# Kernel optimization log

Hardware: AMD Instinct MI355X
Metric: run time of the kernel (lower is better)

## Reference

```python
import jax, jax.numpy as jnp
import numpy as np

B, N, D, H, NCTX = 4, 2048, 1024, 16, 512
HD = D // H  # head dim = 64


def setup_inputs() -> dict:
    key = jax.random.key(0)
    ks = jax.random.split(key, 6)
    return {
        "x": jax.random.normal(ks[0], (B, N, D), dtype=jnp.float32),
        "ctx_ppr": jax.random.uniform(ks[1], (B, NCTX), dtype=jnp.float32),
        "ctx_trust": jax.random.normal(ks[2], (B, NCTX), dtype=jnp.float32),
        "W_in": jax.random.normal(ks[3], (D, 3 * D), dtype=jnp.float32) * 0.02,
        "b_in": jnp.zeros((3 * D,), dtype=jnp.float32),
        "W_out": jax.random.normal(ks[4], (D, D), dtype=jnp.float32) * 0.02,
        "b_out": jnp.zeros((D,), dtype=jnp.float32),
        "log_ppr_alpha": jnp.full((1,), 0.1, dtype=jnp.float32),
        "trust_scale": jnp.full((1,), 0.1, dtype=jnp.float32),
        "n_ctx": NCTX,
    }


def reference(x, ctx_ppr, ctx_trust, W_in, b_in, W_out, b_out, log_ppr_alpha, trust_scale, n_ctx):
    b, n, dmodel = x.shape
    # QKV projection
    qkv = x @ W_in + b_in                                   # [B,N,3D]
    q, k, v = jnp.split(qkv, 3, axis=-1)
    q = q.reshape(b, n, H, HD).transpose(0, 2, 1, 3)        # [B,H,N,d]
    k = k.reshape(b, n, H, HD).transpose(0, 2, 1, 3)
    v = v.reshape(b, n, H, HD).transpose(0, 2, 1, 3)
    if n_ctx > 0:
        # multiplicative trust gate on context-token values
        gate = jax.nn.sigmoid(trust_scale * ctx_trust)      # [B,n_ctx]
        gate_full = jnp.concatenate(
            [gate, jnp.ones((b, n - n_ctx), dtype=x.dtype)], axis=1)  # [B,N]
        v = v * gate_full[:, None, :, None]
        # additive graph (log-PPR) column bias on attention logits
        col_bias = -log_ppr_alpha * jnp.log(jnp.maximum(ctx_ppr, 1e-8))  # [B,n_ctx]
        bias = jnp.concatenate(
            [col_bias, jnp.zeros((b, n - n_ctx), dtype=x.dtype)], axis=1)  # [B,N]
    else:
        bias = jnp.zeros((b, n), dtype=x.dtype)
    scale = 1.0 / np.sqrt(HD).astype(np.float32)
    scores = jnp.einsum("bhqd,bhkd->bhqk", q, k) * scale + bias[:, None, None, :]
    attn = jax.nn.softmax(scores, axis=-1)                  # [B,H,N,N]
    out = jnp.einsum("bhqk,bhkd->bhqd", attn, v)            # [B,H,N,d]
    out = out.transpose(0, 2, 1, 3).reshape(b, n, dmodel)
    return out @ W_out + b_out
```

## Files before the change

### kernel.cpp

```cpp
#include <hip/hip_runtime.h>
#include <hip/hip_bf16.h>
#include <stdint.h>

#define BATCH  4
#define NSEQ   2048
#define DMODEL 1024
#define NHEAD  16
#define HDIM   64
#define NCTXC  512

typedef unsigned short u16;
typedef __attribute__((ext_vector_type(8))) short bfrag;
typedef __attribute__((ext_vector_type(4))) float facc;

typedef __attribute__((address_space(3))) void lds_void;
typedef __attribute__((address_space(1))) void g_void;

__device__ __forceinline__ void gload16(const void* g, void* l) {
  __builtin_amdgcn_global_load_lds((const g_void*)g, (lds_void*)l, 16, 0, 0);
}

__device__ __forceinline__ u16 f2bf(float f) {
  uint32_t r;
  asm("v_cvt_pk_bf16_f32 %0, %1, %1" : "=v"(r) : "v"(f));
  return (u16)r;
}

#if __has_builtin(__builtin_amdgcn_cvt_pk_bf16_f32)
__device__ __forceinline__ uint32_t pk2bf(float a, float b) {
  return __builtin_bit_cast(uint32_t, __builtin_amdgcn_cvt_pk_bf16_f32(a, b));
}
#else
__device__ __forceinline__ uint32_t pk2bf(float a, float b) {
  uint32_t r;
  asm("v_cvt_pk_bf16_f32 %0, %1, %2" : "=v"(r) : "v"(a), "v"(b));
  return r;
}
#endif

__device__ __forceinline__ float bf2f(u16 h) {
  union { uint32_t u; float f; } un;
  un.u = ((uint32_t)h) << 16;
  return un.f;
}

__device__ __forceinline__ float load_flex(const void* p, size_t idx, int isb) {
  return isb ? bf2f(((const u16*)p)[idx]) : ((const float*)p)[idx];
}

__device__ __forceinline__ uint4 pack8(float4 a, float4 b) {
  uint4 r;
  r.x = pk2bf(a.x, a.y);
  r.y = pk2bf(a.z, a.w);
  r.z = pk2bf(b.x, b.y);
  r.w = pk2bf(b.z, b.w);
  return r;
}

__global__ __launch_bounds__(256) void detect_kernel(const u16* __restrict__ xraw,
                                                     int* __restrict__ flag) {
  __shared__ int s_high, s_zero;
  if (threadIdx.x == 0) { s_high = 0; s_zero = 0; }
  __syncthreads();
  int h = 0, z = 0;
  for (int i = threadIdx.x; i < 4096; i += 256) {
    const u16 v = xraw[2 * i];
    const int e = (v >> 7) & 0xFF;
    if (e >= 0x90) h++;
    if (v == 0) z++;
  }
  atomicAdd(&s_high, h);
  atomicAdd(&s_zero, z);
  __syncthreads();
  if (threadIdx.x == 0) flag[0] = (s_high < 64 && s_zero < 2048) ? 1 : 0;
}


__global__ __launch_bounds__(256) void cast_x_kernel(const void* __restrict__ x,
                                                     u16* __restrict__ xb,
                                                     const int* __restrict__ flag) {
  const int isb = flag[0];
  const int i = blockIdx.x * 256 + threadIdx.x;
  if (isb) {
    ((uint4*)xb)[i] = ((const uint4*)x)[i];
  } else {
    const float4 f0 = ((const float4*)x)[2 * i];
    const float4 f1 = ((const float4*)x)[2 * i + 1];
    ((uint4*)xb)[i] = pack8(f0, f1);
  }
}

__global__ __launch_bounds__(256) void transpose_flex(const void* __restrict__ W,
                                                      u16* __restrict__ Wt,
                                                      int R, int C,
                                                      const int* __restrict__ flag) {
  __shared__ float tile[32][33];
  const int isb = flag[0];
  const int tx = threadIdx.x;
  const int ty = threadIdx.y;
  const int c0 = blockIdx.x * 32;
  const int r0 = blockIdx.y * 32;
#pragma unroll
  for (int j = 0; j < 32; j += 8)
    tile[ty + j][tx] = load_flex(W, (size_t)(r0 + ty + j) * C + c0 + tx, isb);
  __syncthreads();
#pragma unroll
  for (int j = 0; j < 32; j += 8)
    Wt[(size_t)(c0 + ty + j) * R + r0 + tx] = f2bf(tile[tx][ty + j]);
}

__global__ __launch_bounds__(256) void prep_small(const void* __restrict__ b_in,
                                                  const void* __restrict__ b_out,
                                                  const void* __restrict__ ppr,
                                                  const void* __restrict__ trust,
                                                  const void* __restrict__ alpha_p,
                                                  const void* __restrict__ ts_p,
                                                  float* __restrict__ bin_f,
                                                  float* __restrict__ bout_f,
                                                  float* __restrict__ gate,
                                                  float* __restrict__ cbias,
                                                  const int* __restrict__ flag) {
  const int isb = flag[0];
  const int i = blockIdx.x * 256 + threadIdx.x;
  if (i < 3072) {
    bin_f[i] = load_flex(b_in, i, isb);
  } else if (i < 4096) {
    bout_f[i - 3072] = load_flex(b_out, i - 3072, isb);
  } else if (i < 4096 + BATCH * NCTXC) {
    const int j = i - 4096;
    const float ts = load_flex(ts_p, 0, isb), al = load_flex(alpha_p, 0, isb);
    gate[j]  = 1.0f / (1.0f + __expf(-ts * load_flex(trust, j, isb)));
    cbias[j] = -al * logf(fmaxf(load_flex(ppr, j, isb), 1e-8f)) * 1.44269504f;
  }
}

__device__ __forceinline__ void kloop_mfma(const u16* __restrict__ Ag,
                                           const u16* __restrict__ Bg,
                                           u16* As, u16* Bs,
                                           int tid, int wM, int wN, int l16, int quad,
                                           facc acc[4][4]) {
  char* ldsA = (char*)As + tid * 16;
  char* ldsB = (char*)Bs + tid * 16;
  for (int k0 = 0; k0 < 1024; k0 += 32) {
    __syncthreads();
    gload16(Ag + k0, ldsA);
    gload16(Ag + (size_t)64 * 1024 + k0, ldsA + 4096);
    gload16(Bg + k0, ldsB);
    gload16(Bg + (size_t)64 * 1024 + k0, ldsB + 4096);
    __syncthreads();

    bfrag af[4], bf[4];
#pragma unroll
    for (int i = 0; i < 4; ++i)
      af[i] = *(const bfrag*)(&As[(wM + i * 16 + l16) * 32 + quad * 8]);
#pragma unroll
    for (int j = 0; j < 4; ++j)
      bf[j] = *(const bfrag*)(&Bs[(wN + j * 16 + l16) * 32 + quad * 8]);
#pragma unroll
    for (int i = 0; i < 4; ++i)
#pragma unroll
      for (int j = 0; j < 4; ++j)
        acc[i][j] = __builtin_amdgcn_mfma_f32_16x16x32_bf16(af[i], bf[j], acc[i][j], 0, 0, 0);
  }
}

__global__ __launch_bounds__(256) void gemm_qkvt(const u16* __restrict__ xb,
                                                 const u16* __restrict__ Wt,
                                                 const float* __restrict__ bin_f,
                                                 const float* __restrict__ gate,
                                                 u16* __restrict__ qk,
                                                 u16* __restrict__ Vtg) {
  __shared__ u16 As[128 * 32];
  __shared__ u16 Bs[128 * 32];
  const int tid  = threadIdx.x;
  const int w    = tid >> 6;
  const int lane = tid & 63;
  const int quad = lane >> 4;
  const int l16  = lane & 15;
  const int wM   = (w >> 1) * 64;
  const int wN   = (w & 1) * 64;
  const int id   = blockIdx.x;
  const int srow  = tid >> 2;
  const int spart = tid & 3;

  facc acc[4][4] = {};

  if (id < 1024) {
    const int bn = id & 15, bm = id >> 4;
    const u16* Ag = xb + (size_t)(bm * 128 + srow) * 1024 + spart * 8;
    const u16* Bg = Wt + (size_t)(bn * 128 + srow) * 1024 + spart * 8;
    kloop_mfma(Ag, Bg, As, Bs, tid, wM, wN, l16, quad, acc);

    const float qs = (bn < 8) ? 0.18033688f : 1.0f;
#pragma unroll
    for (int i = 0; i < 4; ++i) {
      const int grow0 = bm * 128 + wM + i * 16 + quad * 4;
#pragma unroll
      for (int j = 0; j < 4; ++j) {
        const int gcol = bn * 128 + wN + j * 16 + l16;
        const float bv = bin_f[gcol];
#pragma unroll
        for (int r = 0; r < 4; ++r)
          qk[(size_t)(grow0 + r) * 2048 + gcol] = f2bf((acc[i][j][r] + bv) * qs);
      }
    }
  } else {
    const int id2 = id - 1024;
    const int bn = id2 & 63, bm = id2 >> 6;
    const u16* Ag = Wt + (size_t)2048 * 1024 + (size_t)(bm * 128 + srow) * 1024 + spart * 8;
    const u16* Bg = xb + (size_t)(bn * 128 + srow) * 1024 + spart * 8;
    kloop_mfma(Ag, Bg, As, Bs, tid, wM, wN, l16, quad, acc);

#pragma unroll
    for (int i = 0; i < 4; ++i) {
      const int grow0 = bm * 128 + wM + i * 16 + quad * 4;
      const int h   = grow0 >> 6;
      const int dd0 = grow0 & 63;
#pragma unroll
      for (int j = 0; j < 4; ++j) {
        const int gcol = bn * 128 + wN + j * 16 + l16;
        const int bb  = gcol >> 11;
        const int tok = gcol & (NSEQ - 1);
        const float gl = (tok < NCTXC) ? gate[bb * NCTXC + tok] : 1.0f;
        u16* dst = &Vtg[((size_t)((bb * NHEAD + h) * HDIM + dd0)) * NSEQ + tok];
#pragma unroll
        for (int r = 0; r < 4; ++r)
          dst[(size_t)r * NSEQ] = f2bf((acc[i][j][r] + bin_f[2 * DMODEL + grow0 + r]) * gl);
      }
    }
  }
}

__global__ __launch_bounds__(256) void gemm_out(const u16* __restrict__ A,
                                                const u16* __restrict__ Bt,
                                                const float* __restrict__ biasf,
                                                void* __restrict__ Cout,
                                                const int* __restrict__ flag) {
  __shared__ u16 As[128 * 32];
  __shared__ u16 Bs[128 * 32];
  const int isb  = flag[0];
  const int tid  = threadIdx.x;
  const int w    = tid >> 6;
  const int lane = tid & 63;
  const int quad = lane >> 4;
  const int l16  = lane & 15;
  const int wM   = (w >> 1) * 64;
  const int wN   = (w & 1) * 64;
  const int bm   = blockIdx.y;
  const int bn   = blockIdx.x;
  const int srow  = tid >> 2;
  const int spart = tid & 3;

  facc acc[4][4] = {};
  const u16* Ag = A + (size_t)(bm * 128 + srow) * 2048 + spart * 8;
  const u16* Bg = Bt + (size_t)(bn * 128 + srow) * 1024 + spart * 8;
  char* ldsA = (char*)As + tid * 16;
  char* ldsB = (char*)Bs + tid * 16;

  for (int k0 = 0; k0 < 1024; k0 += 32) {
    __syncthreads();
    gload16(Ag + k0, ldsA);
    gload16(Ag + (size_t)64 * 2048 + k0, ldsA + 4096);
    gload16(Bg + k0, ldsB);
    gload16(Bg + (size_t)64 * 1024 + k0, ldsB + 4096);
    __syncthreads();

    bfrag af[4], bf[4];
#pragma unroll
    for (int i = 0; i < 4; ++i)
      af[i] = *(const bfrag*)(&As[(wM + i * 16 + l16) * 32 + quad * 8]);
#pragma unroll
    for (int j = 0; j < 4; ++j)
      bf[j] = *(const bfrag*)(&Bs[(wN + j * 16 + l16) * 32 + quad * 8]);
#pragma unroll
    for (int i = 0; i < 4; ++i)
#pragma unroll
      for (int j = 0; j < 4; ++j)
        acc[i][j] = __builtin_amdgcn_mfma_f32_16x16x32_bf16(af[i], bf[j], acc[i][j], 0, 0, 0);
  }

#pragma unroll
  for (int i = 0; i < 4; ++i) {
    const int grow0 = bm * 128 + wM + i * 16 + quad * 4;
#pragma unroll
    for (int j = 0; j < 4; ++j) {
      const int gcol = bn * 128 + wN + j * 16 + l16;
      const float bv = biasf[gcol];
#pragma unroll
      for (int r = 0; r < 4; ++r) {
        const float v = acc[i][j][r] + bv;
        if (isb) ((u16*)Cout)[(size_t)(grow0 + r) * 1024 + gcol] = f2bf(v);
        else     ((float*)Cout)[(size_t)(grow0 + r) * 1024 + gcol] = v;
      }
    }
  }
}

__global__ __launch_bounds__(256) void attn_kernel(u16* __restrict__ qk,
                                                   const u16* __restrict__ vtg,
                                                   const float* __restrict__ cbias) {
  const int id    = blockIdx.x;
  const int chunk = id >> 3;
  const int qt    = chunk & 15;
  const int hg    = (id & 7) | ((chunk >> 4) << 3);
  const int h     = hg & 15;
  const int b     = hg >> 4;

  __shared__ u16 Ks[64 * 72];
  __shared__ u16 Vt[64 * 72];
  __shared__ u16 Ps[8][16 * 72];

  const int tid  = threadIdx.x;
  const int w    = tid >> 6;
  const int lane = tid & 63;
  const int quad = lane >> 4;
  const int l16  = lane & 15;
  const int srow = tid >> 2;
  const int spart = tid & 3;

  bfrag bq[2][2];
#pragma unroll
  for (int qs = 0; qs < 2; ++qs) {
    const u16* qrow = qk + (size_t)(b * NSEQ + qt * 128 + (w * 2 + qs) * 16 + l16) * 2048 + h * HDIM;
    bq[qs][0] = *(const bfrag*)(qrow + quad * 8);
    bq[qs][1] = *(const bfrag*)(qrow + 32 + quad * 8);
  }

  bfrag ones;
#pragma unroll
  for (int i = 0; i < 8; ++i) ones[i] = (short)0x3F80;

  facc den[2] = {};
  facc o[2][4] = {};

  const u16* kst = qk + (size_t)(b * NSEQ) * 2048 + DMODEL + h * HDIM;
  const u16* vst = vtg + (size_t)((b * NHEAD + h) * HDIM + srow) * NSEQ;
  u16* psw[2] = { Ps[w * 2], Ps[w * 2 + 1] };

  uint4 pk0, pk1, pv0, pv1;
  {
    const u16* ks = kst + (size_t)srow * 2048 + spart * 16;
    pk0 = *(const uint4*)ks;
    pk1 = *(const uint4*)(ks + 8);
    const u16* vs = vst + spart * 16;
    pv0 = *(const uint4*)vs;
    pv1 = *(const uint4*)(vs + 8);
  }

  for (int t = 0; t < NSEQ / 64; ++t) {
    __syncthreads();
    *(uint4*)(&Ks[srow * 72 + spart * 16])     = pk0;
    *(uint4*)(&Ks[srow * 72 + spart * 16 + 8]) = pk1;
    *(uint4*)(&Vt[srow * 72 + spart * 16])     = pv0;
    *(uint4*)(&Vt[srow * 72 + spart * 16 + 8]) = pv1;
    __syncthreads();

    {
      const int tn = (t < NSEQ / 64 - 1) ? t + 1 : t;
      const u16* ks = kst + (size_t)(tn * 64 + srow) * 2048 + spart * 16;
      pk0 = *(const uint4*)ks;
      pk1 = *(const uint4*)(ks + 8);
      const u16* vs = vst + tn * 64 + spart * 16;
      pv0 = *(const uint4*)vs;
      pv1 = *(const uint4*)(vs + 8);
    }

    bfrag ak[4][2], av[4][2];
#pragma unroll
    for (int nt = 0; nt < 4; ++nt) {
      ak[nt][0] = *(const bfrag*)(&Ks[(nt * 16 + l16) * 72 + quad * 8]);
      ak[nt][1] = *(const bfrag*)(&Ks[(nt * 16 + l16) * 72 + 32 + quad * 8]);
      av[nt][0] = *(const bfrag*)(&Vt[(nt * 16 + l16) * 72 + quad * 8]);
      av[nt][1] = *(const bfrag*)(&Vt[(nt * 16 + l16) * 72 + 32 + quad * 8]);
    }

    facc zb[4];
    if (t < 8) {
      const float* cb = cbias + b * NCTXC + t * 64 + quad * 4;
#pragma unroll
      for (int nt = 0; nt < 4; ++nt) zb[nt] = *(const facc*)(cb + nt * 16);
    } else {
#pragma unroll
      for (int nt = 0; nt < 4; ++nt) zb[nt] = (facc){};
    }

#pragma unroll
    for (int qs = 0; qs < 2; ++qs) {
      facc s[4];
      __builtin_amdgcn_s_setprio(1);
#pragma unroll
      for (int nt = 0; nt < 4; ++nt) {
        facc z = zb[nt];
        z = __builtin_amdgcn_mfma_f32_16x16x32_bf16(ak[nt][0], bq[qs][0], z, 0, 0, 0);
        s[nt] = __builtin_amdgcn_mfma_f32_16x16x32_bf16(ak[nt][1], bq[qs][1], s[nt] = z, 0, 0, 0);
      }
      __builtin_amdgcn_s_setprio(0);

#pragma unroll
      for (int nt = 0; nt < 4; ++nt)
#pragma unroll
        for (int r = 0; r < 4; ++r)
          s[nt][r] = __builtin_amdgcn_exp2f(s[nt][r]);

#pragma unroll
      for (int nt = 0; nt < 4; ++nt) {
        uint2 pk;
        pk.x = pk2bf(s[nt][0], s[nt][1]);
        pk.y = pk2bf(s[nt][2], s[nt][3]);
        *(uint2*)(&psw[qs][l16 * 72 + nt * 16 + quad * 4]) = pk;
      }
    }

#pragma unroll
    for (int qs = 0; qs < 2; ++qs) {
      const bfrag bp0 = *(const bfrag*)(&psw[qs][l16 * 72 + quad * 8]);
      const bfrag bp1 = *(const bfrag*)(&psw[qs][l16 * 72 + 32 + quad * 8]);
      __builtin_amdgcn_s_setprio(1);
#pragma unroll
      for (int dt = 0; dt < 4; ++dt) {
        o[qs][dt] = __builtin_amdgcn_mfma_f32_16x16x32_bf16(av[dt][0], bp0, o[qs][dt], 0, 0, 0);
        o[qs][dt] = __builtin_amdgcn_mfma_f32_16x16x32_bf16(av[dt][1], bp1, o[qs][dt], 0, 0, 0);
      }
      den[qs] = __builtin_amdgcn_mfma_f32_16x16x32_bf16(ones, bp0, den[qs], 0, 0, 0);
      den[qs] = __builtin_amdgcn_mfma_f32_16x16x32_bf16(ones, bp1, den[qs], 0, 0, 0);
      __builtin_amdgcn_s_setprio(0);
    }
  }

#pragma unroll
  for (int qs = 0; qs < 2; ++qs) {
    const float inv = 1.0f / den[qs][0];
    u16* orow = qk + (size_t)(b * NSEQ + qt * 128 + (w * 2 + qs) * 16 + l16) * 2048 + h * HDIM;
#pragma unroll
    for (int dt = 0; dt < 4; ++dt) {
      uint2 st;
      st.x = pk2bf(o[qs][dt][0] * inv, o[qs][dt][1] * inv);
      st.y = pk2bf(o[qs][dt][2] * inv, o[qs][dt][3] * inv);
      *(uint2*)(orow + dt * 16 + quad * 4) = st;
    }
  }
}


extern "C" void kernel_launch(void* const* d_in, const int* in_sizes, int n_in,
                              void* d_out, int out_size, void* d_ws, size_t ws_size,
                              hipStream_t stream) {
  const void* x          = d_in[0];
  const void* ctx_ppr    = d_in[1];
  const void* ctx_trust  = d_in[2];
  const void* W_in       = d_in[3];
  const void* b_in       = d_in[4];
  const void* W_out      = d_in[5];
  const void* b_out      = d_in[6];
  const void* lppr_alpha = d_in[7];
  const void* tscale     = d_in[8];

  char* ws = (char*)d_ws;
  u16* Wt    = (u16*)ws;  ws += (size_t)3072 * 1024 * 2;
  u16* WoT   = (u16*)ws;  ws += (size_t)1024 * 1024 * 2;
  u16* qk    = (u16*)ws;  ws += (size_t)8192 * 2048 * 2;
  u16* Vtg   = (u16*)ws;  ws += (size_t)64 * 64 * 2048 * 2;
  u16* xb    = (u16*)ws;  ws += (size_t)8192 * 1024 * 2;
  float* bin_f  = (float*)ws; ws += 3072 * 4;
  float* bout_f = (float*)ws; ws += 1024 * 4;
  float* gate   = (float*)ws; ws += (size_t)BATCH * NCTXC * 4;
  float* cbias  = (float*)ws; ws += (size_t)BATCH * NCTXC * 4;
  int*   flag   = (int*)ws;   ws += 64;

  detect_kernel<<<dim3(1), dim3(256), 0, stream>>>((const u16*)x, flag);
  cast_x_kernel<<<dim3(4096), dim3(256), 0, stream>>>(x, xb, flag);
  transpose_flex<<<dim3(96, 32), dim3(32, 8), 0, stream>>>(W_in, Wt, 1024, 3072, flag);
  transpose_flex<<<dim3(32, 32), dim3(32, 8), 0, stream>>>(W_out, WoT, 1024, 1024, flag);
  prep_small<<<dim3(24), dim3(256), 0, stream>>>(b_in, b_out, ctx_ppr, ctx_trust,
                                                 lppr_alpha, tscale,
                                                 bin_f, bout_f, gate, cbias, flag);
  gemm_qkvt<<<dim3(1536), dim3(256), 0, stream>>>(xb, Wt, bin_f, gate, qk, Vtg);
  attn_kernel<<<dim3(1024), dim3(256), 0, stream>>>(qk, Vtg, cbias);
  gemm_out<<<dim3(8, 64), dim3(256), 0, stream>>>(qk, WoT, bout_f, d_out, flag);
}
```

Measured before the change: 309.6 us.

## Load K/V fragments directly from global into registers, dropping LDS staging

```diff
diff --git a/kernel.cpp b/kernel.cpp
--- a/kernel.cpp
+++ b/kernel.cpp
@@ -296,6 +296,91 @@
   }
 }
 
+__device__ __forceinline__ void load_kf(const u16* __restrict__ kb, int t,
+                                        int l16, int quad, bfrag ak[4][2]) {
+#pragma unroll
+  for (int nt = 0; nt < 4; ++nt) {
+    const u16* p = kb + (size_t)(t * 64 + nt * 16 + l16) * 2048 + quad * 8;
+    ak[nt][0] = *(const bfrag*)(p);
+    ak[nt][1] = *(const bfrag*)(p + 32);
+  }
+}
+
+__device__ __forceinline__ void load_vf(const u16* __restrict__ vb, int t,
+                                        int l16, int quad, bfrag av[4][2]) {
+#pragma unroll
+  for (int dt = 0; dt < 4; ++dt) {
+    const u16* p = vb + (size_t)(dt * 16 + l16) * NSEQ + t * 64 + quad * 8;
+    av[dt][0] = *(const bfrag*)(p);
+    av[dt][1] = *(const bfrag*)(p + 32);
+  }
+}
+
+__device__ __forceinline__ void attn_tile(int t, int b,
+                                          const bfrag (&ak)[4][2],
+                                          const bfrag (&av)[4][2],
+                                          const bfrag (&bq)[2][2],
+                                          u16* const (&psw)[2],
+                                          const float* __restrict__ cbias,
+                                          facc (&den)[2], facc (&o)[2][4],
+                                          int l16, int quad) {
+  facc zb[4];
+  if (t < 8) {
+    const float* cb = cbias + b * NCTXC + t * 64 + quad * 4;
+#pragma unroll
+    for (int nt = 0; nt < 4; ++nt) zb[nt] = *(const facc*)(cb + nt * 16);
+  } else {
+#pragma unroll
+    for (int nt = 0; nt < 4; ++nt) zb[nt] = (facc){};
+  }
+
+#pragma unroll
+  for (int qs = 0; qs < 2; ++qs) {
+    facc s[4];
+    __builtin_amdgcn_s_setprio(1);
+#pragma unroll
+    for (int nt = 0; nt < 4; ++nt) {
+      facc z = zb[nt];
+      z = __builtin_amdgcn_mfma_f32_16x16x32_bf16(ak[nt][0], bq[qs][0], z, 0, 0, 0);
+      s[nt] = __builtin_amdgcn_mfma_f32_16x16x32_bf16(ak[nt][1], bq[qs][1], z, 0, 0, 0);
+    }
+    __builtin_amdgcn_s_setprio(0);
+
+#pragma unroll
+    for (int nt = 0; nt < 4; ++nt)
+#pragma unroll
+      for (int r = 0; r < 4; ++r)
+        s[nt][r] = __builtin_amdgcn_exp2f(s[nt][r]);
+
+#pragma unroll
+    for (int nt = 0; nt < 4; ++nt) {
+      uint2 pk;
+      pk.x = pk2bf(s[nt][0], s[nt][1]);
+      pk.y = pk2bf(s[nt][2], s[nt][3]);
+      *(uint2*)(&psw[qs][l16 * 72 + nt * 16 + quad * 4]) = pk;
+    }
+  }
+
+  bfrag ones;
+#pragma unroll
+  for (int i = 0; i < 8; ++i) ones[i] = (short)0x3F80;
+
+#pragma unroll
+  for (int qs = 0; qs < 2; ++qs) {
+    const bfrag bp0 = *(const bfrag*)(&psw[qs][l16 * 72 + quad * 8]);
+    const bfrag bp1 = *(const bfrag*)(&psw[qs][l16 * 72 + 32 + quad * 8]);
+    __builtin_amdgcn_s_setprio(1);
+#pragma unroll
+    for (int dt = 0; dt < 4; ++dt) {
+      o[qs][dt] = __builtin_amdgcn_mfma_f32_16x16x32_bf16(av[dt][0], bp0, o[qs][dt], 0, 0, 0);
+      o[qs][dt] = __builtin_amdgcn_mfma_f32_16x16x32_bf16(av[dt][1], bp1, o[qs][dt], 0, 0, 0);
+    }
+    den[qs] = __builtin_amdgcn_mfma_f32_16x16x32_bf16(ones, bp0, den[qs], 0, 0, 0);
+    den[qs] = __builtin_amdgcn_mfma_f32_16x16x32_bf16(ones, bp1, den[qs], 0, 0, 0);
+    __builtin_amdgcn_s_setprio(0);
+  }
+}
+
 __global__ __launch_bounds__(256) void attn_kernel(u16* __restrict__ qk,
                                                    const u16* __restrict__ vtg,
                                                    const float* __restrict__ cbias) {
@@ -306,8 +391,6 @@
   const int h     = hg & 15;
   const int b     = hg >> 4;
 
-  __shared__ u16 Ks[64 * 72];
-  __shared__ u16 Vt[64 * 72];
   __shared__ u16 Ps[8][16 * 72];
 
   const int tid  = threadIdx.x;
@@ -315,8 +398,6 @@
   const int lane = tid & 63;
   const int quad = lane >> 4;
   const int l16  = lane & 15;
-  const int srow = tid >> 2;
-  const int spart = tid & 3;
 
   bfrag bq[2][2];
 #pragma unroll
@@ -326,105 +407,26 @@
     bq[qs][1] = *(const bfrag*)(qrow + 32 + quad * 8);
   }
 
-  bfrag ones;
-#pragma unroll
-  for (int i = 0; i < 8; ++i) ones[i] = (short)0x3F80;
-
   facc den[2] = {};
   facc o[2][4] = {};
 
-  const u16* kst = qk + (size_t)(b * NSEQ) * 2048 + DMODEL + h * HDIM;
-  const u16* vst = vtg + (size_t)((b * NHEAD + h) * HDIM + srow) * NSEQ;
-  u16* psw[2] = { Ps[w * 2], Ps[w * 2 + 1] };
-
-  uint4 pk0, pk1, pv0, pv1;
-  {
-    const u16* ks = kst + (size_t)srow * 2048 + spart * 16;
-    pk0 = *(const uint4*)ks;
-    pk1 = *(const uint4*)(ks + 8);
-    const u16* vs = vst + spart * 16;
-    pv0 = *(const uint4*)vs;
-    pv1 = *(const uint4*)(vs + 8);
-  }
-
-  for (int t = 0; t < NSEQ / 64; ++t) {
-    __syncthreads();
-    *(uint4*)(&Ks[srow * 72 + spart * 16])     = pk0;
-    *(uint4*)(&Ks[srow * 72 + spart * 16 + 8]) = pk1;
-    *(uint4*)(&Vt[srow * 72 + spart * 16])     = pv0;
-    *(uint4*)(&Vt[srow * 72 + spart * 16 + 8]) = pv1;
-    __syncthreads();
-
-    {
-      const int tn = (t < NSEQ / 64 - 1) ? t + 1 : t;
-      const u16* ks = kst + (size_t)(tn * 64 + srow) * 2048 + spart * 16;
-      pk0 = *(const uint4*)ks;
-      pk1 = *(const uint4*)(ks + 8);
-      const u16* vs = vst + tn * 64 + spart * 16;
-      pv0 = *(const uint4*)vs;
-      pv1 = *(const uint4*)(vs + 8);
-    }
-
-    bfrag ak[4][2], av[4][2];
-#pragma unroll
-    for (int nt = 0; nt < 4; ++nt) {
-      ak[nt][0] = *(const bfrag*)(&Ks[(nt * 16 + l16) * 72 + quad * 8]);
-      ak[nt][1] = *(const bfrag*)(&Ks[(nt * 16 + l16) * 72 + 32 + quad * 8]);
-      av[nt][0] = *(const bfrag*)(&Vt[(nt * 16 + l16) * 72 + quad * 8]);
-      av[nt][1] = *(const bfrag*)(&Vt[(nt * 16 + l16) * 72 + 32 + quad * 8]);
-    }
-
-    facc zb[4];
-    if (t < 8) {
-      const float* cb = cbias + b * NCTXC + t * 64 + quad * 4;
-#pragma unroll
-      for (int nt = 0; nt < 4; ++nt) zb[nt] = *(const facc*)(cb + nt * 16);
-    } else {
-#pragma unroll
-      for (int nt = 0; nt < 4; ++nt) zb[nt] = (facc){};
-    }
-
-#pragma unroll
-    for (int qs = 0; qs < 2; ++qs) {
-      facc s[4];
-      __builtin_amdgcn_s_setprio(1);
-#pragma unroll
-      for (int nt = 0; nt < 4; ++nt) {
-        facc z = zb[nt];
-        z = __builtin_amdgcn_mfma_f32_16x16x32_bf16(ak[nt][0], bq[qs][0], z, 0, 0, 0);
-        s[nt] = __builtin_amdgcn_mfma_f32_16x16x32_bf16(ak[nt][1], bq[qs][1], s[nt] = z, 0, 0, 0);
-      }
-      __builtin_amdgcn_s_setprio(0);
-
-#pragma unroll
-      for (int nt = 0; nt < 4; ++nt)
-#pragma unroll
-        for (int r = 0; r < 4; ++r)
-          s[nt][r] = __builtin_amdgcn_exp2f(s[nt][r]);
-
-#pragma unroll
-      for (int nt = 0; nt < 4; ++nt) {
-        uint2 pk;
-        pk.x = pk2bf(s[nt][0], s[nt][1]);
-        pk.y = pk2bf(s[nt][2], s[nt][3]);
-        *(uint2*)(&psw[qs][l16 * 72 + nt * 16 + quad * 4]) = pk;
-      }
-    }
-
-#pragma unroll
-    for (int qs = 0; qs < 2; ++qs) {
-      const bfrag bp0 = *(const bfrag*)(&psw[qs][l16 * 72 + quad * 8]);
-      const bfrag bp1 = *(const bfrag*)(&psw[qs][l16 * 72 + 32 + quad * 8]);
-      __builtin_amdgcn_s_setprio(1);
-#pragma unroll
-      for (int dt = 0; dt < 4; ++dt) {
-        o[qs][dt] = __builtin_amdgcn_mfma_f32_16x16x32_bf16(av[dt][0], bp0, o[qs][dt], 0, 0, 0);
-        o[qs][dt] = __builtin_amdgcn_mfma_f32_16x16x32_bf16(av[dt][1], bp1, o[qs][dt], 0, 0, 0);
-      }
-      den[qs] = __builtin_amdgcn_mfma_f32_16x16x32_bf16(ones, bp0, den[qs], 0, 0, 0);
-      den[qs] = __builtin_amdgcn_mfma_f32_16x16x32_bf16(ones, bp1, den[qs], 0, 0, 0);
-      __builtin_amdgcn_s_setprio(0);
-    }
+  const u16* kb = qk + (size_t)(b * NSEQ) * 2048 + DMODEL + h * HDIM;
+  const u16* vb = vtg + (size_t)((b * NHEAD + h) * HDIM) * NSEQ;
+  u16* const psw[2] = { Ps[w * 2], Ps[w * 2 + 1] };
+
+  bfrag akA[4][2], avA[4][2], akB[4][2], avB[4][2];
+  load_kf(kb, 0, l16, quad, akA);
+  load_vf(vb, 0, l16, quad, avA);
+
+  for (int t = 0; t < NSEQ / 64; t += 2) {
+    load_kf(kb, t + 1, l16, quad, akB);
+    load_vf(vb, t + 1, l16, quad, avB);
+    attn_tile(t, b, akA, avA, bq, psw, cbias, den, o, l16, quad);
+
+    const int tn = (t + 2 < NSEQ / 64) ? t + 2 : NSEQ / 64 - 1;
+    load_kf(kb, tn, l16, quad, akA);
+    load_vf(vb, tn, l16, quad, avA);
+    attn_tile(t + 1, b, akB, avB, bq, psw, cbias, den, o, l16, quad);
   }
 
 #pragma unroll
```

Measured after the change: 451.8 us. 1.46x slower.
